# Performance work log

Measured on AMD Instinct MI355X. Metric: run time of the kernel, lower is better.

The kernel has to match this reference:

```python
import jax, jax.numpy as jnp
import numpy as np

B, T, D_IN, H, N_CLASSES = 32, 64, 10000, 200, 2


def setup_inputs() -> dict:
    key = jax.random.key(0)
    ks = jax.random.split(key, 16)
    s_in = 1.0 / np.sqrt(H)  # torch nn.RNN init scale
    def u(k, shape):
        return jax.random.uniform(k, shape, jnp.float32, -s_in, s_in)
    inp = {"x": jax.random.normal(ks[0], (B, T, D_IN), jnp.float32)}
    dims = [D_IN, H, H]
    for l in range(3):
        inp[f"W_ih{l}"] = u(ks[1 + 4 * l], (H, dims[l]))
        inp[f"W_hh{l}"] = u(ks[2 + 4 * l], (H, H))
        inp[f"b_ih{l}"] = u(ks[3 + 4 * l], (H,))
        inp[f"b_hh{l}"] = u(ks[4 + 4 * l], (H,))
    inp["fc_w"] = u(ks[13], (N_CLASSES, H))
    inp["fc_b"] = u(ks[14], (N_CLASSES,))
    return inp


def _rnn_layer(x_seq, W_ih, W_hh, b_ih, b_hh):
    # x_seq: [B, T, D] -> hidden sequence [B, T, H]
    pre = jnp.einsum('btd,hd->bth', x_seq, W_ih) + b_ih + b_hh  # input proj batched over time
    h0 = jnp.zeros((x_seq.shape[0], W_hh.shape[0]), x_seq.dtype)

    def step(h, p_t):
        h_new = jnp.tanh(p_t + h @ W_hh.T)
        return h_new, h_new

    _, hs = jax.lax.scan(step, h0, jnp.swapaxes(pre, 0, 1))  # [T, B, H]
    return jnp.swapaxes(hs, 0, 1)


def reference(x, W_ih0, W_hh0, b_ih0, b_hh0, W_ih1, W_hh1, b_ih1, b_hh1,
              W_ih2, W_hh2, b_ih2, b_hh2, fc_w, fc_b):
    h = _rnn_layer(x, W_ih0, W_hh0, b_ih0, b_hh0)
    h = _rnn_layer(h, W_ih1, W_hh1, b_ih1, b_hh1)
    h = _rnn_layer(h, W_ih2, W_hh2, b_ih2, b_hh2)
    last = h[:, -1, :]  # [B, H]; dropout is identity at inference
    logits = last @ fc_w.T + fc_b  # [B, n_classes]
    return logits
```

## Files before the change

kernel.cpp:

```cpp
#include <hip/hip_runtime.h>
#include <hip/hip_bf16.h>


typedef __bf16  bf16x8 __attribute__((ext_vector_type(8)));
typedef __bf16  bf16x4 __attribute__((ext_vector_type(4)));
typedef float   f32x4  __attribute__((ext_vector_type(4)));

#define HDIM 200
#define BM 64
#define CHUNK_B 26624
#define MFMA(a, b, c) __builtin_amdgcn_mfma_f32_16x16x32_bf16(a, b, c, 0, 0, 0)

__device__ __forceinline__ void glds16(const void* g, void* l) {
    __builtin_amdgcn_global_load_lds(
        (const __attribute__((address_space(1))) unsigned int*)g,
        (__attribute__((address_space(3))) unsigned int*)l, 16, 0, 0);
}

__global__ void pack_all(const float* __restrict__ W0,
                         const float* __restrict__ W1,
                         const float* __restrict__ W2,
                         __bf16* __restrict__ O0,
                         __bf16* __restrict__ O1,
                         __bf16* __restrict__ O2)
{
    const int T0 = 320 * 1664, T1 = 7 * 1664, T2 = 7 * 1664;
    for (int gt = blockIdx.x * blockDim.x + threadIdx.x; gt < T0 + T1 + T2;
         gt += gridDim.x * blockDim.x) {
        const float* W; __bf16* out; int K, g;
        if (gt < T0)           { W = W0; out = O0; K = 10000; g = gt; }
        else if (gt < T0 + T1) { W = W1; out = O1; K = HDIM;  g = gt - T0; }
        else                   { W = W2; out = O2; K = HDIM;  g = gt - T0 - T1; }

        const int kc = g / 1664;
        const int u  = g - kc * 1664;
        const int isLo = (u >= 832);
        const int u2 = isLo ? u - 832 : u;
        const int nt = u2 >> 6;
        const int l  = u2 & 63;
        const int r  = nt * 16 + (l & 15);
        const int k  = kc * 32 + (l >> 4) * 8;
        bf16x8 v;
        if (r < HDIM && k < K) {
            const float* p = W + (size_t)r * K + k;
            float4 a = *(const float4*)p, b = *(const float4*)(p + 4);
            float f[8] = {a.x, a.y, a.z, a.w, b.x, b.y, b.z, b.w};
#pragma unroll
            for (int i = 0; i < 8; ++i) {
                __bf16 h = (__bf16)f[i];
                v[i] = isLo ? (__bf16)(f[i] - (float)h) : h;
            }
        } else {
#pragma unroll
            for (int i = 0; i < 8; ++i) v[i] = (__bf16)0.f;
        }
        *(bf16x8*)&out[(size_t)g * 8] = v;
    }
}

__global__ __launch_bounds__(512, 4)
void gemm_pipe(const float* __restrict__ A, int lda, int K,
               const __bf16* __restrict__ Bpack,
               float* __restrict__ Cbase, int per_split, int ksteps)
{
    __shared__ alignas(16) __bf16 Ab[2][4096];
    __shared__ alignas(16) __bf16 Bb[2][13312];

    const int tid = threadIdx.x;
    const int kc0 = blockIdx.y * ksteps;
    const int m0  = blockIdx.x * BM;
    float* __restrict__ C = Cbase + (size_t)blockIdx.y * per_split;

    const int wv = tid >> 6, lane = tid & 63;
    const int r16 = lane & 15, kg = lane >> 4;
    const int mg = wv & 1, ng = wv >> 1;
    const int nt0 = ng ? 1 + ng * 3 : 0;
    const int ntw = ng ? 3 : 4;
    const int fb  = lane * 8;

    const int a_row = tid >> 3;
    const int a_q   = tid & 7;
    const float* Arow = A + (size_t)(m0 + a_row) * lda + a_q * 4;
    const int a_off = (a_row >> 4) * 512 + ((a_row & 15) + 16 * (a_q >> 1)) * 8
                    + (a_q & 1) * 4;

    f32x4 acc[2][4];
#pragma unroll
    for (int mi = 0; mi < 2; ++mi)
#pragma unroll
        for (int j = 0; j < 4; ++j) acc[mi][j] = (f32x4)0.f;

    float av[4];
    auto loadA = [&](int ks) {
        const int kb = (kc0 + ks) * 32;
        if (kb + a_q * 4 < K) {
            float4 x0 = *(const float4*)(Arow + kb);
            av[0] = x0.x; av[1] = x0.y; av[2] = x0.z; av[3] = x0.w;
        } else {
#pragma unroll
            for (int i = 0; i < 4; ++i) av[i] = 0.f;
        }
    };
    auto issueB = [&](int ks, int buf) {
        const char* src = (const char*)Bpack + (size_t)(kc0 + ks) * CHUNK_B;
        char* dst = (char*)&Bb[buf][0];
#pragma unroll
        for (int r = 0; r < 3; ++r)
            glds16(src + (r * 512 + tid) * 16, dst + (r * 512 + tid) * 16);
        if (tid < 128)
            glds16(src + (1536 + tid) * 16, dst + (1536 + tid) * 16);
    };

    loadA(0);
    issueB(0, 0);

    for (int ks = 0; ks < ksteps; ++ks) {
        const int cur = ks & 1, nxt = cur ^ 1;
        bf16x4 th, tl;
#pragma unroll
        for (int i = 0; i < 4; ++i) {
            __bf16 h = (__bf16)av[i];
            th[i] = h; tl[i] = (__bf16)(av[i] - (float)h);
        }
        *(bf16x4*)&Ab[cur][a_off]        = th;
        *(bf16x4*)&Ab[cur][2048 + a_off] = tl;
        __syncthreads();
        if (ks + 1 < ksteps) { issueB(ks + 1, nxt); loadA(ks + 1); }

        const int ao0 = (mg * 2 + 0) * 512 + fb;
        const int ao1 = (mg * 2 + 1) * 512 + fb;
        bf16x8 ah0 = *(const bf16x8*)&Ab[cur][ao0];
        bf16x8 al0 = *(const bf16x8*)&Ab[cur][2048 + ao0];
        bf16x8 ah1 = *(const bf16x8*)&Ab[cur][ao1];
        bf16x8 al1 = *(const bf16x8*)&Ab[cur][2048 + ao1];
#pragma unroll
        for (int j = 0; j < 4; ++j) {
            if (j < ntw) {
                const int bo = (nt0 + j) * 512 + fb;
                bf16x8 bh = *(const bf16x8*)&Bb[cur][bo];
                bf16x8 bl = *(const bf16x8*)&Bb[cur][6656 + bo];
                acc[0][j] = MFMA(al0, bh, acc[0][j]);
                acc[0][j] = MFMA(ah0, bl, acc[0][j]);
                acc[0][j] = MFMA(ah0, bh, acc[0][j]);
                acc[1][j] = MFMA(al1, bh, acc[1][j]);
                acc[1][j] = MFMA(ah1, bl, acc[1][j]);
                acc[1][j] = MFMA(ah1, bh, acc[1][j]);
            }
        }
    }

#pragma unroll
    for (int mi = 0; mi < 2; ++mi) {
        const int rb = m0 + mg * 32 + mi * 16 + kg * 4;
#pragma unroll
        for (int j = 0; j < 4; ++j) {
            if (j < ntw) {
                const int n = (nt0 + j) * 16 + r16;
                if (n < HDIM)
#pragma unroll
                    for (int r = 0; r < 4; ++r)
                        C[(size_t)(rb + r) * HDIM + n] = acc[mi][j][r];
            }
        }
    }
}

__global__ void reduce_parts(const float* __restrict__ Pp, float* __restrict__ P)
{
    const int i = blockIdx.x * blockDim.x + threadIdx.x;
    if (i < 102400) {
        float4 s = ((const float4*)Pp)[i];
#pragma unroll
        for (int r = 1; r < 16; ++r) {
            float4 v = ((const float4*)Pp)[(size_t)r * 102400 + i];
            s.x += v.x; s.y += v.y; s.z += v.z; s.w += v.w;
        }
        ((float4*)P)[i] = s;
    }
}

__device__ __forceinline__ float fast_tanh(float x) {
    float e = __expf(-2.f * fabsf(x));
    float r = (1.f - e) / (1.f + e);
    return copysignf(r, x);
}

__device__ __forceinline__ void bar_lds() {
    asm volatile("s_waitcnt lgkmcnt(0)" ::: "memory");
    __builtin_amdgcn_s_barrier();
}

__global__ __launch_bounds__(512, 1)
void rnn_rec(const float* __restrict__ pre,
             const float* __restrict__ Whh,
             const float* __restrict__ bih,
             const float* __restrict__ bhh,
             float* __restrict__ Hout)
{
    const int b   = blockIdx.x;
    const int tid = threadIdx.x;

    __shared__ float preS[64 * HDIM];
    __shared__ float h[HDIM];
    __shared__ float bias[HDIM];
    __shared__ float part[10][HDIM];

    {
        const float4* ps = (const float4*)(pre + (size_t)b * 64 * HDIM);
        float4* pd = (float4*)preS;
        for (int i = tid; i < 3200; i += 512) pd[i] = ps[i];
    }

    const bool act = tid < 500;
    const int g  = tid / 10;
    const int s  = tid - g * 10;
    const int n0 = g * 4;
    const int k0 = s * 20;

    float w[80];
    if (act) {
#pragma unroll
        for (int j = 0; j < 4; ++j) {
            const float* wr = Whh + (size_t)(n0 + j) * HDIM + k0;
#pragma unroll
            for (int i = 0; i < 5; ++i) {
                float4 v = *(const float4*)(wr + i * 4);
                w[j * 20 + i * 4 + 0] = v.x; w[j * 20 + i * 4 + 1] = v.y;
                w[j * 20 + i * 4 + 2] = v.z; w[j * 20 + i * 4 + 3] = v.w;
            }
        }
    }
    if (tid < HDIM) { bias[tid] = bih[tid] + bhh[tid]; h[tid] = 0.f; }
    __syncthreads();

    for (int t = 0; t < 64; ++t) {
        if (act) {
            float a0 = 0.f, a1 = 0.f, a2 = 0.f, a3 = 0.f;
#pragma unroll
            for (int i = 0; i < 5; ++i) {
                float4 hv = *(const float4*)&h[k0 + i * 4];
                a0 += w[ 0 + i*4]*hv.x + w[ 1 + i*4]*hv.y + w[ 2 + i*4]*hv.z + w[ 3 + i*4]*hv.w;
                a1 += w[20 + i*4]*hv.x + w[21 + i*4]*hv.y + w[22 + i*4]*hv.z + w[23 + i*4]*hv.w;
                a2 += w[40 + i*4]*hv.x + w[41 + i*4]*hv.y + w[42 + i*4]*hv.z + w[43 + i*4]*hv.w;
                a3 += w[60 + i*4]*hv.x + w[61 + i*4]*hv.y + w[62 + i*4]*hv.z + w[63 + i*4]*hv.w;
            }
            float4 pv = make_float4(a0, a1, a2, a3);
            *(float4*)&part[s][n0] = pv;
        }
        bar_lds();
        if (tid < HDIM) {
            float sum = part[0][tid];
#pragma unroll
            for (int r = 1; r < 10; ++r) sum += part[r][tid];
            float v = fast_tanh(sum + preS[t * HDIM + tid] + bias[tid]);
            h[tid] = v;
            Hout[((size_t)b * 64 + t) * HDIM + tid] = v;
        }
        bar_lds();
    }
}

__global__ void fc_head(const float* __restrict__ Hlast_base,
                        const float* __restrict__ fcw,
                        const float* __restrict__ fcb,
                        float* __restrict__ out)
{
    const int i = threadIdx.x;
    if (i >= 64) return;
    const int b = i >> 1, cls = i & 1;
    const float* hp = Hlast_base + ((size_t)b * 64 + 63) * HDIM;
    const float* fw = fcw + cls * HDIM;
    float s = fcb[cls];
    for (int j = 0; j < HDIM; ++j) s += hp[j] * fw[j];
    out[b * 2 + cls] = s;
}

extern "C" void kernel_launch(void* const* d_in, const int* in_sizes, int n_in,
                              void* d_out, int out_size, void* d_ws, size_t ws_size,
                              hipStream_t stream) {
    const float* x     = (const float*)d_in[0];
    const float* W_ih0 = (const float*)d_in[1];
    const float* W_hh0 = (const float*)d_in[2];
    const float* b_ih0 = (const float*)d_in[3];
    const float* b_hh0 = (const float*)d_in[4];
    const float* W_ih1 = (const float*)d_in[5];
    const float* W_hh1 = (const float*)d_in[6];
    const float* b_ih1 = (const float*)d_in[7];
    const float* b_hh1 = (const float*)d_in[8];
    const float* W_ih2 = (const float*)d_in[9];
    const float* W_hh2 = (const float*)d_in[10];
    const float* b_ih2 = (const float*)d_in[11];
    const float* b_hh2 = (const float*)d_in[12];
    const float* fc_w  = (const float*)d_in[13];
    const float* fc_b  = (const float*)d_in[14];
    float* out = (float*)d_out;

    const size_t PE = (size_t)2048 * HDIM;
    float* P     = (float*)d_ws;
    float* Hbuf  = P + PE;
    float* Hbuf2 = Hbuf + PE;
    float* Ppart = Hbuf2 + PE;
    __bf16* W0p  = (__bf16*)(Ppart + 16 * PE);
    __bf16* W1p  = W0p + (size_t)320 * 13312;
    __bf16* W2p  = W1p + (size_t)7 * 13312;

    pack_all<<<1024, 256, 0, stream>>>(W_ih0, W_ih1, W_ih2, W0p, W1p, W2p);

    gemm_pipe<<<dim3(32, 16), 512, 0, stream>>>(x, 10000, 10000, W0p, Ppart, (int)PE, 20);
    reduce_parts<<<400, 256, 0, stream>>>(Ppart, P);
    rnn_rec<<<32, 512, 0, stream>>>(P, W_hh0, b_ih0, b_hh0, Hbuf);

    gemm_pipe<<<dim3(32, 1), 512, 0, stream>>>(Hbuf, HDIM, HDIM, W1p, P, (int)PE, 7);
    rnn_rec<<<32, 512, 0, stream>>>(P, W_hh1, b_ih1, b_hh1, Hbuf2);

    gemm_pipe<<<dim3(32, 1), 512, 0, stream>>>(Hbuf2, HDIM, HDIM, W2p, P, (int)PE, 7);
    rnn_rec<<<32, 512, 0, stream>>>(P, W_hh2, b_ih2, b_hh2, Hbuf);

    fc_head<<<1, 64, 0, stream>>>(Hbuf, fc_w, fc_b, out);
}
```

Measured before the change: 315.5 us.

## Compute recurrent h@W_hh with split-bf16 MFMA instead of scalar FP32 FMAs

The recurrent kernel now packs W_hh into split-precision bf16 (hi/lo) MFMA fragments in the shared pack kernel. Each step multiplies h by W_hh with three MFMAs per K-chunk, which removes the per-step partial-sum array and the 10-way cross-thread reduction. The goal is a shorter serial per-timestep latency across 64 steps in three layers. The costs are extra MFMA work, since only row 0 of each 16x16 tile is useful, a 3-term bf16 split that only approximates FP32, and a larger pack kernel.

```diff
diff --git a/kernel.cpp b/kernel.cpp
--- a/kernel.cpp
+++ b/kernel.cpp
@@ -17,20 +17,47 @@
         (__attribute__((address_space(3))) unsigned int*)l, 16, 0, 0);
 }
 
-__global__ void pack_all(const float* __restrict__ W0,
-                         const float* __restrict__ W1,
-                         const float* __restrict__ W2,
-                         __bf16* __restrict__ O0,
-                         __bf16* __restrict__ O1,
-                         __bf16* __restrict__ O2)
-{
-    const int T0 = 320 * 1664, T1 = 7 * 1664, T2 = 7 * 1664;
-    for (int gt = blockIdx.x * blockDim.x + threadIdx.x; gt < T0 + T1 + T2;
+__device__ __forceinline__ float fast_tanh(float x) {
+    float e = __expf(-2.f * fabsf(x));
+    float r = (1.f - e) / (1.f + e);
+    return copysignf(r, x);
+}
+
+__device__ __forceinline__ void bar_lds() {
+    asm volatile("s_waitcnt lgkmcnt(0)" ::: "memory");
+    __builtin_amdgcn_s_barrier();
+}
+
+__global__ void pack_all(const float* __restrict__ Wi0,
+                         const float* __restrict__ Wi1,
+                         const float* __restrict__ Wi2,
+                         const float* __restrict__ Wh0,
+                         const float* __restrict__ Wh1,
+                         const float* __restrict__ Wh2,
+                         __bf16* __restrict__ Oi0,
+                         __bf16* __restrict__ Oi1,
+                         __bf16* __restrict__ Oi2,
+                         __bf16* __restrict__ Oh0,
+                         __bf16* __restrict__ Oh1,
+                         __bf16* __restrict__ Oh2)
+{
+    const int T0 = 320 * 1664, TS = 7 * 1664;
+    const int total = T0 + 5 * TS;
+    for (int gt = blockIdx.x * blockDim.x + threadIdx.x; gt < total;
          gt += gridDim.x * blockDim.x) {
         const float* W; __bf16* out; int K, g;
-        if (gt < T0)           { W = W0; out = O0; K = 10000; g = gt; }
-        else if (gt < T0 + T1) { W = W1; out = O1; K = HDIM;  g = gt - T0; }
-        else                   { W = W2; out = O2; K = HDIM;  g = gt - T0 - T1; }
+        if (gt < T0)               { W = Wi0; out = Oi0; K = 10000; g = gt; }
+        else {
+            int r5 = gt - T0;
+            int which = r5 / TS;   g = r5 - which * TS;  K = HDIM;
+            switch (which) {
+                case 0: W = Wi1; out = Oi1; break;
+                case 1: W = Wi2; out = Oi2; break;
+                case 2: W = Wh0; out = Oh0; break;
+                case 3: W = Wh1; out = Oh1; break;
+                default: W = Wh2; out = Oh2; break;
+            }
+        }
 
         const int kc = g / 1664;
         const int u  = g - kc * 1664;
@@ -179,82 +206,74 @@
     }
 }
 
-__device__ __forceinline__ float fast_tanh(float x) {
-    float e = __expf(-2.f * fabsf(x));
-    float r = (1.f - e) / (1.f + e);
-    return copysignf(r, x);
-}
-
-__device__ __forceinline__ void bar_lds() {
-    asm volatile("s_waitcnt lgkmcnt(0)" ::: "memory");
-    __builtin_amdgcn_s_barrier();
-}
-
 __global__ __launch_bounds__(512, 1)
-void rnn_rec(const float* __restrict__ pre,
-             const float* __restrict__ Whh,
-             const float* __restrict__ bih,
-             const float* __restrict__ bhh,
-             float* __restrict__ Hout)
+void rnn_recM(const float* __restrict__ pre,
+              const __bf16* __restrict__ WhhP,
+              const float* __restrict__ bih,
+              const float* __restrict__ bhh,
+              float* __restrict__ Hout)
 {
     const int b   = blockIdx.x;
     const int tid = threadIdx.x;
 
     __shared__ float preS[64 * HDIM];
-    __shared__ float h[HDIM];
     __shared__ float bias[HDIM];
-    __shared__ float part[10][HDIM];
+    __shared__ __bf16 hSh[224];
+    __shared__ __bf16 hSl[224];
 
     {
         const float4* ps = (const float4*)(pre + (size_t)b * 64 * HDIM);
         float4* pd = (float4*)preS;
         for (int i = tid; i < 3200; i += 512) pd[i] = ps[i];
     }
-
-    const bool act = tid < 500;
-    const int g  = tid / 10;
-    const int s  = tid - g * 10;
-    const int n0 = g * 4;
-    const int k0 = s * 20;
-
-    float w[80];
-    if (act) {
-#pragma unroll
-        for (int j = 0; j < 4; ++j) {
-            const float* wr = Whh + (size_t)(n0 + j) * HDIM + k0;
-#pragma unroll
-            for (int i = 0; i < 5; ++i) {
-                float4 v = *(const float4*)(wr + i * 4);
-                w[j * 20 + i * 4 + 0] = v.x; w[j * 20 + i * 4 + 1] = v.y;
-                w[j * 20 + i * 4 + 2] = v.z; w[j * 20 + i * 4 + 3] = v.w;
-            }
-        }
-    }
-    if (tid < HDIM) { bias[tid] = bih[tid] + bhh[tid]; h[tid] = 0.f; }
+    if (tid < HDIM) bias[tid] = bih[tid] + bhh[tid];
+    if (tid < 224) { hSh[tid] = (__bf16)0.f; hSl[tid] = (__bf16)0.f; }
+
+    const int wv = tid >> 6, lane = tid & 63, kg = lane >> 4;
+    const int ntA = wv;
+    const int ntB = wv + 8;
+    const int ntBc = ntB < 13 ? ntB : 12;
+
+    const __bf16* bA = WhhP + ((size_t)ntA  * 64 + lane) * 8;
+    const __bf16* bB = WhhP + ((size_t)ntBc * 64 + lane) * 8;
+#define LW(KC) \
+    const bf16x8 wAh##KC = *(const bf16x8*)(bA + KC * 13312); \
+    const bf16x8 wAl##KC = *(const bf16x8*)(bA + KC * 13312 + 6656); \
+    const bf16x8 wBh##KC = *(const bf16x8*)(bB + KC * 13312); \
+    const bf16x8 wBl##KC = *(const bf16x8*)(bB + KC * 13312 + 6656);
+    LW(0) LW(1) LW(2) LW(3) LW(4) LW(5) LW(6)
+#undef LW
     __syncthreads();
 
     for (int t = 0; t < 64; ++t) {
-        if (act) {
-            float a0 = 0.f, a1 = 0.f, a2 = 0.f, a3 = 0.f;
-#pragma unroll
-            for (int i = 0; i < 5; ++i) {
-                float4 hv = *(const float4*)&h[k0 + i * 4];
-                a0 += w[ 0 + i*4]*hv.x + w[ 1 + i*4]*hv.y + w[ 2 + i*4]*hv.z + w[ 3 + i*4]*hv.w;
-                a1 += w[20 + i*4]*hv.x + w[21 + i*4]*hv.y + w[22 + i*4]*hv.z + w[23 + i*4]*hv.w;
-                a2 += w[40 + i*4]*hv.x + w[41 + i*4]*hv.y + w[42 + i*4]*hv.z + w[43 + i*4]*hv.w;
-                a3 += w[60 + i*4]*hv.x + w[61 + i*4]*hv.y + w[62 + i*4]*hv.z + w[63 + i*4]*hv.w;
-            }
-            float4 pv = make_float4(a0, a1, a2, a3);
-            *(float4*)&part[s][n0] = pv;
-        }
+        f32x4 aA0 = (f32x4)0.f, aA1 = (f32x4)0.f;
+        f32x4 aB0 = (f32x4)0.f, aB1 = (f32x4)0.f;
+#define RK(KC, SA, SB) { \
+        const bf16x8 hh = *(const bf16x8*)&hSh[KC * 32 + kg * 8]; \
+        const bf16x8 hl = *(const bf16x8*)&hSl[KC * 32 + kg * 8]; \
+        SA = MFMA(hl, wAh##KC, SA); SA = MFMA(hh, wAl##KC, SA); \
+        SA = MFMA(hh, wAh##KC, SA); \
+        SB = MFMA(hl, wBh##KC, SB); SB = MFMA(hh, wBl##KC, SB); \
+        SB = MFMA(hh, wBh##KC, SB); }
+        RK(0, aA0, aB0) RK(1, aA1, aB1) RK(2, aA0, aB0) RK(3, aA1, aB1)
+        RK(4, aA0, aB0) RK(5, aA1, aB1) RK(6, aA0, aB0)
+#undef RK
+        const float rA = aA0[0] + aA1[0];
+        const float rB = aB0[0] + aB1[0];
         bar_lds();
-        if (tid < HDIM) {
-            float sum = part[0][tid];
-#pragma unroll
-            for (int r = 1; r < 10; ++r) sum += part[r][tid];
-            float v = fast_tanh(sum + preS[t * HDIM + tid] + bias[tid]);
-            h[tid] = v;
-            Hout[((size_t)b * 64 + t) * HDIM + tid] = v;
+        if (lane < 16) {
+            const int nA = ntA * 16 + lane;
+            float v = fast_tanh(rA + preS[t * HDIM + nA] + bias[nA]);
+            __bf16 vh = (__bf16)v;
+            hSh[nA] = vh; hSl[nA] = (__bf16)(v - (float)vh);
+            Hout[((size_t)b * 64 + t) * HDIM + nA] = v;
+            const int nB = ntB * 16 + lane;
+            if (nB < HDIM) {
+                float v2 = fast_tanh(rB + preS[t * HDIM + nB] + bias[nB]);
+                __bf16 vh2 = (__bf16)v2;
+                hSh[nB] = vh2; hSl[nB] = (__bf16)(v2 - (float)vh2);
+                Hout[((size_t)b * 64 + t) * HDIM + nB] = v2;
+            }
         }
         bar_lds();
     }
@@ -296,25 +315,31 @@
     float* out = (float*)d_out;
 
     const size_t PE = (size_t)2048 * HDIM;
+    const size_t CH = (size_t)7 * 13312;
     float* P     = (float*)d_ws;
     float* Hbuf  = P + PE;
     float* Hbuf2 = Hbuf + PE;
     float* Ppart = Hbuf2 + PE;
     __bf16* W0p  = (__bf16*)(Ppart + 16 * PE);
     __bf16* W1p  = W0p + (size_t)320 * 13312;
-    __bf16* W2p  = W1p + (size_t)7 * 13312;
-
-    pack_all<<<1024, 256, 0, stream>>>(W_ih0, W_ih1, W_ih2, W0p, W1p, W2p);
+    __bf16* W2p  = W1p + CH;
+    __bf16* Wh0p = W2p + CH;
+    __bf16* Wh1p = Wh0p + CH;
+    __bf16* Wh2p = Wh1p + CH;
+
+    pack_all<<<1024, 256, 0, stream>>>(W_ih0, W_ih1, W_ih2,
+                                       W_hh0, W_hh1, W_hh2,
+                                       W0p, W1p, W2p, Wh0p, Wh1p, Wh2p);
 
     gemm_pipe<<<dim3(32, 16), 512, 0, stream>>>(x, 10000, 10000, W0p, Ppart, (int)PE, 20);
     reduce_parts<<<400, 256, 0, stream>>>(Ppart, P);
-    rnn_rec<<<32, 512, 0, stream>>>(P, W_hh0, b_ih0, b_hh0, Hbuf);
+    rnn_recM<<<32, 512, 0, stream>>>(P, Wh0p, b_ih0, b_hh0, Hbuf);
 
     gemm_pipe<<<dim3(32, 1), 512, 0, stream>>>(Hbuf, HDIM, HDIM, W1p, P, (int)PE, 7);
-    rnn_rec<<<32, 512, 0, stream>>>(P, W_hh1, b_ih1, b_hh1, Hbuf2);
+    rnn_recM<<<32, 512, 0, stream>>>(P, Wh1p, b_ih1, b_hh1, Hbuf2);
 
     gemm_pipe<<<dim3(32, 1), 512, 0, stream>>>(Hbuf2, HDIM, HDIM, W2p, P, (int)PE, 7);
-    rnn_rec<<<32, 512, 0, stream>>>(P, W_hh2, b_ih2, b_hh2, Hbuf);
+    rnn_recM<<<32, 512, 0, stream>>>(P, Wh2p, b_ih2, b_hh2, Hbuf);
 
     fc_head<<<1, 64, 0, stream>>>(Hbuf, fc_w, fc_b, out);
 }
```

Measured after the change: 391.8 us. 1.24x slower.
